# Performance work log

Measured on AMD Instinct MI355X. Metric: run time of the kernel, lower is better.

Reference implementation:

```python
import jax, jax.numpy as jnp
import numpy as np

B, S, D, H, FF = 4, 2048, 512, 8, 2048
HD = D // H
WINDOW = 64  # local attention half-window in rank space
EPS = 1e-5


def _layer_norm(v, g, b):
    m = jnp.mean(v, axis=-1, keepdims=True)
    var = jnp.mean(jnp.square(v - m), axis=-1, keepdims=True)
    return (v - m) / jnp.sqrt(var + EPS) * g + b


def setup_inputs() -> dict:
    key = jax.random.key(0)
    ks = jax.random.split(key, 10)
    sc = 0.02
    x = jax.random.normal(ks[0], (B, S, D), jnp.float32)
    padding_mask = jnp.zeros((B, S), dtype=bool)
    i = jnp.arange(S)
    local = jnp.abs(i[:, None] - i[None, :]) <= WINDOW
    glob = (i[:, None] == 0) | (i[None, :] == 0)  # global spectrum token at pos 0
    attn_mask = jnp.where(local | glob, 0.0, -jnp.inf).astype(jnp.float32)
    return {
        "x": x,
        "padding_mask": padding_mask,
        "attn_mask": attn_mask,
        "in_proj_w": jax.random.normal(ks[1], (3 * D, D), jnp.float32) * sc,
        "in_proj_b": jnp.zeros((3 * D,), jnp.float32),
        "out_proj_w": jax.random.normal(ks[2], (D, D), jnp.float32) * sc,
        "out_proj_b": jnp.zeros((D,), jnp.float32),
        "ln1_g": jnp.ones((D,), jnp.float32),
        "ln1_b": jnp.zeros((D,), jnp.float32),
        "ln2_g": jnp.ones((D,), jnp.float32),
        "ln2_b": jnp.zeros((D,), jnp.float32),
        "ff_w1": jax.random.normal(ks[3], (FF, D), jnp.float32) * sc,
        "ff_b1": jnp.zeros((FF,), jnp.float32),
        "ff_w2": jax.random.normal(ks[4], (D, FF), jnp.float32) * sc,
        "ff_b2": jnp.zeros((D,), jnp.float32),
    }


def reference(x, padding_mask, attn_mask, in_proj_w, in_proj_b, out_proj_w,
              out_proj_b, ln1_g, ln1_b, ln2_g, ln2_b, ff_w1, ff_b1, ff_w2, ff_b2):
    # pre-LN attention
    a = _layer_norm(x, ln1_g, ln1_b)
    qkv = a @ in_proj_w.T + in_proj_b  # [B,S,3D]
    q, k, v = jnp.split(qkv, 3, axis=-1)
    to_heads = lambda t: t.reshape(B, S, H, HD).transpose(0, 2, 1, 3)
    q, k, v = to_heads(q), to_heads(k), to_heads(v)
    scores = jnp.einsum('bhqd,bhkd->bhqk', q, k) * (HD ** -0.5)
    # float attn_mask path: key_padding_mask converted to additive -inf floats
    kpm = jnp.where(padding_mask, -jnp.inf, 0.0).astype(scores.dtype)
    scores = scores + attn_mask[None, None, :, :] + kpm[:, None, None, :]
    p = jax.nn.softmax(scores, axis=-1)
    o = jnp.einsum('bhqk,bhkd->bhqd', p, v).transpose(0, 2, 1, 3).reshape(B, S, D)
    o = o @ out_proj_w.T + out_proj_b
    x = x + o  # residual (dropout = 0)
    # pre-LN feed-forward with exact GELU (torch nn.GELU default)
    f = _layer_norm(x, ln2_g, ln2_b)
    f = jax.nn.gelu(f @ ff_w1.T + ff_b1, approximate=False) @ ff_w2.T + ff_b2
    return x + f
```

## Files before the change

kernel.cpp:

```cpp
#include <hip/hip_runtime.h>
#include <hip/hip_bf16.h>
#include <math.h>

namespace {

constexpr int kB = 4, kS = 2048, kD = 512, kH = 8, kFF = 2048;
constexpr int kM = kB * kS;
constexpr int kHD = kD / kH;
constexpr int kWin = 64;

typedef __attribute__((ext_vector_type(8))) short short8;
typedef __attribute__((ext_vector_type(4))) float f32x4;

__device__ __forceinline__ float bf2f(__hip_bfloat16 v) { return __bfloat162float(v); }
__device__ __forceinline__ __hip_bfloat16 f2bf(float v) { return __float2bfloat16(v); }
__device__ __forceinline__ int iclamp(int v, int lo, int hi) { return v < lo ? lo : (v > hi ? hi : v); }

__device__ __forceinline__ void async16(const void* g, void* l) {
  __builtin_amdgcn_global_load_lds((const __attribute__((address_space(1))) void*)g,
                                   (__attribute__((address_space(3))) void*)l, 16, 0, 0);
}

__global__ __launch_bounds__(256)
void prep(const float* __restrict__ iw, const float* __restrict__ ow,
          const float* __restrict__ f1, const float* __restrict__ f2,
          __hip_bfloat16* __restrict__ wq, __hip_bfloat16* __restrict__ wo,
          __hip_bfloat16* __restrict__ w1, __hip_bfloat16* __restrict__ w2,
          const float* __restrict__ x, const float* __restrict__ g,
          const float* __restrict__ bta, __hip_bfloat16* __restrict__ a,
          __hip_bfloat16* __restrict__ xb) {
  const int id = blockIdx.x;
  if (id < 3072) {
    const float* s; __hip_bfloat16* d; int base;
    if (id < 768)       { s = iw; d = wq; base = id; }
    else if (id < 1024) { s = ow; d = wo; base = id - 768; }
    else if (id < 2048) { s = f1; d = w1; base = id - 1024; }
    else                { s = f2; d = w2; base = id - 2048; }
    int i = base * 1024 + threadIdx.x * 4;
    float4 v = *(const float4*)(s + i);
    union { __hip_bfloat16 h[4]; uint2 u; } t;
    t.h[0] = f2bf(v.x); t.h[1] = f2bf(v.y); t.h[2] = f2bf(v.z); t.h[3] = f2bf(v.w);
    *(uint2*)(d + i) = t.u;
  } else {
    int row = (id - 3072) * 4 + (threadIdx.x >> 6);
    int lane = threadIdx.x & 63;
    const float* xr = x + (size_t)row * kD;
    int c = lane * 8;
    float4 v0 = *(const float4*)(xr + c);
    float4 v1 = *(const float4*)(xr + c + 4);
    union { __hip_bfloat16 h[8]; int4 u; } xr8;
    xr8.h[0] = f2bf(v0.x); xr8.h[1] = f2bf(v0.y); xr8.h[2] = f2bf(v0.z); xr8.h[3] = f2bf(v0.w);
    xr8.h[4] = f2bf(v1.x); xr8.h[5] = f2bf(v1.y); xr8.h[6] = f2bf(v1.z); xr8.h[7] = f2bf(v1.w);
    *(int4*)(xb + (size_t)row * kD + c) = xr8.u;
    float s  = v0.x + v0.y + v0.z + v0.w + v1.x + v1.y + v1.z + v1.w;
    float ss = v0.x*v0.x + v0.y*v0.y + v0.z*v0.z + v0.w*v0.w
             + v1.x*v1.x + v1.y*v1.y + v1.z*v1.z + v1.w*v1.w;
#pragma unroll
    for (int o = 32; o > 0; o >>= 1) { s += __shfl_xor(s, o); ss += __shfl_xor(ss, o); }
    float mean = s * (1.0f / kD);
    float inv  = rsqrtf(ss * (1.0f / kD) - mean * mean + 1e-5f);
    float4 g0 = *(const float4*)(g + c),   g1 = *(const float4*)(g + c + 4);
    float4 b0 = *(const float4*)(bta + c), b1 = *(const float4*)(bta + c + 4);
    union { __hip_bfloat16 h[8]; int4 u; } t;
    t.h[0] = f2bf((v0.x - mean) * inv * g0.x + b0.x);
    t.h[1] = f2bf((v0.y - mean) * inv * g0.y + b0.y);
    t.h[2] = f2bf((v0.z - mean) * inv * g0.z + b0.z);
    t.h[3] = f2bf((v0.w - mean) * inv * g0.w + b0.w);
    t.h[4] = f2bf((v1.x - mean) * inv * g1.x + b1.x);
    t.h[5] = f2bf((v1.y - mean) * inv * g1.y + b1.y);
    t.h[6] = f2bf((v1.z - mean) * inv * g1.z + b1.z);
    t.h[7] = f2bf((v1.w - mean) * inv * g1.w + b1.w);
    *(int4*)(a + (size_t)row * kD + c) = t.u;
  }
}

__global__ __launch_bounds__(256)
void ln_rows_bf(const __hip_bfloat16* __restrict__ x, const float* __restrict__ g,
                const float* __restrict__ bta, __hip_bfloat16* __restrict__ out) {
  int row = blockIdx.x * 4 + (threadIdx.x >> 6);
  int lane = threadIdx.x & 63;
  int c = lane * 8;
  union { short8 v; __hip_bfloat16 hh[8]; } u;
  u.v = *(const short8*)(x + (size_t)row * kD + c);
  float f[8];
  float s = 0.f, ss = 0.f;
#pragma unroll
  for (int i = 0; i < 8; ++i) { f[i] = bf2f(u.hh[i]); s += f[i]; ss += f[i] * f[i]; }
#pragma unroll
  for (int o = 32; o > 0; o >>= 1) { s += __shfl_xor(s, o); ss += __shfl_xor(ss, o); }
  float mean = s * (1.0f / kD);
  float inv  = rsqrtf(ss * (1.0f / kD) - mean * mean + 1e-5f);
  float4 g0 = *(const float4*)(g + c),   g1 = *(const float4*)(g + c + 4);
  float4 b0 = *(const float4*)(bta + c), b1 = *(const float4*)(bta + c + 4);
  union { __hip_bfloat16 h[8]; int4 v; } t;
  t.h[0] = f2bf((f[0] - mean) * inv * g0.x + b0.x);
  t.h[1] = f2bf((f[1] - mean) * inv * g0.y + b0.y);
  t.h[2] = f2bf((f[2] - mean) * inv * g0.z + b0.z);
  t.h[3] = f2bf((f[3] - mean) * inv * g0.w + b0.w);
  t.h[4] = f2bf((f[4] - mean) * inv * g1.x + b1.x);
  t.h[5] = f2bf((f[5] - mean) * inv * g1.y + b1.y);
  t.h[6] = f2bf((f[6] - mean) * inv * g1.z + b1.z);
  t.h[7] = f2bf((f[7] - mean) * inv * g1.w + b1.w);
  *(int4*)(out + (size_t)row * kD + c) = t.v;
}

__global__ __launch_bounds__(64)
void attn_tile(const __hip_bfloat16* __restrict__ qkv, const __hip_bfloat16* __restrict__ vt,
               __hip_bfloat16* __restrict__ o) {
  const int bh = blockIdx.x;
  const int b = bh >> 3, h = bh & 7;
  const int lane = threadIdx.x;

  __shared__ float smem_f[2048];
  __shared__ float qs0[kHD];
  __hip_bfloat16* Pt = (__hip_bfloat16*)smem_f;

  const __hip_bfloat16* base = qkv + (size_t)b * kS * (3 * kD);
  const __hip_bfloat16* vt_bh = vt + (size_t)(b * kH + h) * kHD * kS;

  if (blockIdx.y == 0) {
    qs0[lane] = bf2f(base[h * kHD + lane]) * 0.125f;
    __syncthreads();
    float m = -1e30f;
    for (int kk = lane; kk < kS; kk += 64) {
      const short8* kp = (const short8*)(base + (size_t)kk * (3 * kD) + kD + h * kHD);
      float s = 0.f;
#pragma unroll
      for (int cc = 0; cc < 8; ++cc) {
        union { short8 v; __hip_bfloat16 hh[8]; } u;
        u.v = kp[cc];
#pragma unroll
        for (int d = 0; d < 8; ++d) s += qs0[cc * 8 + d] * bf2f(u.hh[d]);
      }
      smem_f[kk] = s;
      m = fmaxf(m, s);
    }
#pragma unroll
    for (int off = 32; off > 0; off >>= 1) m = fmaxf(m, __shfl_xor(m, off));
    float ls = 0.f;
    __syncthreads();
    for (int kk = lane; kk < kS; kk += 64) {
      float e = __expf(smem_f[kk] - m);
      smem_f[kk] = e;
      ls += e;
    }
#pragma unroll
    for (int off = 32; off > 0; off >>= 1) ls += __shfl_xor(ls, off);
    __syncthreads();
    float a = 0.f;
    const __hip_bfloat16* vr = vt_bh + (size_t)lane * kS;
    for (int c = 0; c < kS / 8; ++c) {
      union { short8 v; __hip_bfloat16 hh[8]; } u;
      u.v = *(const short8*)(vr + c * 8);
#pragma unroll
      for (int j = 0; j < 8; ++j) a += smem_f[c * 8 + j] * bf2f(u.hh[j]);
    }
    o[(size_t)(b * kS) * kD + h * kHD + lane] = f2bf(a / ls);
    return;
  }

  const int tq = blockIdx.y - 1;
  const int quad = lane >> 4, col = lane & 15;
  const int q0 = tq * 16;
  const int kbase = q0 - kWin;

  short8 aq0, aq1;
  {
    const __hip_bfloat16* qrow = base + (size_t)(q0 + col) * (3 * kD) + h * kHD + quad * 8;
    aq0 = *(const short8*)qrow;
    aq1 = *(const short8*)(qrow + 32);
  }

  f32x4 sc[10];
#pragma unroll
  for (int t = 0; t < 10; ++t) {
    int krow = (t < 9) ? iclamp(kbase + t * 16 + col, 0, kS - 1) : col;
    const short8* kp = (const short8*)(base + (size_t)krow * (3 * kD) + kD + h * kHD + quad * 8);
    f32x4 a = (f32x4){0.f, 0.f, 0.f, 0.f};
    a = __builtin_amdgcn_mfma_f32_16x16x32_bf16(aq0, kp[0], a, 0, 0, 0);
    a = __builtin_amdgcn_mfma_f32_16x16x32_bf16(aq1, kp[4], a, 0, 0, 0);
    sc[t] = a;
  }

  float rowmax[4] = {-1e30f, -1e30f, -1e30f, -1e30f};
#pragma unroll
  for (int t = 0; t < 10; ++t) {
#pragma unroll
    for (int r = 0; r < 4; ++r) {
      int q = q0 + quad * 4 + r;
      bool valid;
      if (t < 9) {
        int k = kbase + t * 16 + col;
        valid = (k >= 0) && (k < kS) && ((q - k <= kWin && k - q <= kWin) || k == 0);
      } else {
        valid = (col == 0) && (kbase > 0);
      }
      float s = valid ? sc[t][r] * 0.125f : -1e30f;
      sc[t][r] = s;
      rowmax[r] = fmaxf(rowmax[r], s);
    }
  }
#pragma unroll
  for (int r = 0; r < 4; ++r)
#pragma unroll
    for (int off = 1; off < 16; off <<= 1)
      rowmax[r] = fmaxf(rowmax[r], __shfl_xor(rowmax[r], off));

  float rowsum[4] = {0.f, 0.f, 0.f, 0.f};
#pragma unroll
  for (int t = 0; t < 10; ++t)
#pragma unroll
    for (int r = 0; r < 4; ++r) {
      float e = __expf(sc[t][r] - rowmax[r]);
      sc[t][r] = e;
      rowsum[r] += e;
    }
#pragma unroll
  for (int r = 0; r < 4; ++r)
#pragma unroll
    for (int off = 1; off < 16; off <<= 1)
      rowsum[r] += __shfl_xor(rowsum[r], off);

#pragma unroll
  for (int t = 0; t < 10; ++t) {
    union { ushort u[4]; unsigned long long ll; } pk;
#pragma unroll
    for (int r = 0; r < 4; ++r) {
      __hip_bfloat16 hv = f2bf(sc[t][r]);
      pk.u[r] = *(ushort*)&hv;
    }
    *(unsigned long long*)&Pt[(t * 16 + col) * 20 + quad * 4] = pk.ll;
  }
  __syncthreads();

  f32x4 oacc[4];
#pragma unroll
  for (int n = 0; n < 4; ++n) oacc[n] = (f32x4){0.f, 0.f, 0.f, 0.f};

#pragma unroll
  for (int c = 0; c < 5; ++c) {
    union { short s[8]; short8 v; } pa;
#pragma unroll
    for (int j = 0; j < 8; ++j) pa.s[j] = *(const short*)&Pt[(c * 32 + quad * 8 + j) * 20 + col];
    const int kc = c * 32 + quad * 8;
    const int kstart = (kc < 144) ? iclamp(kbase + kc, 0, kS - 8) : (kc - 144);
#pragma unroll
    for (int n = 0; n < 4; ++n) {
      short8 vb = *(const short8*)(vt_bh + (size_t)(n * 16 + col) * kS + kstart);
      oacc[n] = __builtin_amdgcn_mfma_f32_16x16x32_bf16(pa.v, vb, oacc[n], 0, 0, 0);
    }
  }

#pragma unroll
  for (int n = 0; n < 4; ++n)
#pragma unroll
    for (int r = 0; r < 4; ++r) {
      int q = q0 + quad * 4 + r;
      if (q == 0) continue;
      o[(size_t)(b * kS + q) * kD + h * kHD + n * 16 + col] = f2bf(oacc[n][r] / rowsum[r]);
    }
}

template <int TN, int NB, int EPI, int WVT, typename OT, typename RT>
__global__ __launch_bounds__(256, 4)
void gemm_bt(const __hip_bfloat16* __restrict__ A, const __hip_bfloat16* __restrict__ W,
             const float* __restrict__ bias, const RT* __restrict__ resid,
             OT* __restrict__ C, __hip_bfloat16* __restrict__ vt, int Ndim, int K) {
  constexpr int NF = TN / 32;
  __shared__ __hip_bfloat16 As[128 * 64];
  __shared__ __hip_bfloat16 Ws[TN * 64];

  const int id = blockIdx.x;
  const int rr = id & 7, tt = id >> 3;
  const int nb = tt % NB, mb = (tt / NB) * 8 + rr;

  const int tid = threadIdx.x;
  const int lane = tid & 63, w = tid >> 6;
  const int wm = w >> 1, wn = w & 1;
  const int quad = lane >> 4, mrow = lane & 15;
  const int m0 = mb * 128, n0 = nb * TN;

  const int lrow = lane >> 3;
  const int lcol = ((lane & 7) ^ lrow) << 3;

  f32x4 acc[4][NF];
#pragma unroll
  for (int i = 0; i < 4; ++i)
#pragma unroll
    for (int j = 0; j < NF; ++j) acc[i][j] = (f32x4){0.f, 0.f, 0.f, 0.f};

  for (int kt = 0; kt < K; kt += 64) {
#pragma unroll
    for (int it = 0; it < 4; ++it) {
      int c = w * 4 + it;
      async16(A + (size_t)(m0 + c * 8 + lrow) * K + kt + lcol, &As[c * 512]);
    }
#pragma unroll
    for (int it = 0; it < NF; ++it) {
      int c = w * NF + it;
      async16(W + (size_t)(n0 + c * 8 + lrow) * K + kt + lcol, &Ws[c * 512]);
    }
    __syncthreads();
#pragma unroll
    for (int kk = 0; kk < 64; kk += 32) {
      const int ch = (kk >> 3) + quad;
      const int sw = (ch ^ (mrow & 7)) << 3;
      short8 af[4], wf[NF];
#pragma unroll
      for (int i = 0; i < 4; ++i)
        af[i] = *(const short8*)&As[(wm * 64 + i * 16 + mrow) * 64 + sw];
#pragma unroll
      for (int j = 0; j < NF; ++j)
        wf[j] = *(const short8*)&Ws[(wn * (TN / 2) + j * 16 + mrow) * 64 + sw];
#pragma unroll
      for (int i = 0; i < 4; ++i)
#pragma unroll
        for (int j = 0; j < NF; ++j)
          acc[i][j] = __builtin_amdgcn_mfma_f32_16x16x32_bf16(af[i], wf[j], acc[i][j], 0, 0, 0);
    }
    __syncthreads();
  }

  if constexpr (WVT) {
    if (n0 >= 1024) {
      __hip_bfloat16* Ls = As;
      const int bb = m0 >> 11, ss0 = m0 & (kS - 1);
      const int n0v = n0 - 1024;
#pragma unroll
      for (int p = 0; p < 2; ++p) {
        __syncthreads();
#pragma unroll
        for (int jj = 0; jj < 2; ++jj) {
          int j = p * 2 + jj;
          int lr = wn * 32 + jj * 16 + mrow;
          float bs = bias[1024 + n0v + wn * 64 + j * 16 + mrow];
#pragma unroll
          for (int i = 0; i < 4; ++i) {
            int tok = wm * 64 + i * 16 + quad * 4;
            int tw = tok ^ ((lr & 15) << 3);
            union { __hip_bfloat16 h[4]; unsigned long long u; } pk;
#pragma unroll
            for (int r = 0; r < 4; ++r) pk.h[r] = f2bf(acc[i][j][r] + bs);
            *(unsigned long long*)&Ls[lr * 128 + tw] = pk.u;
          }
        }
        __syncthreads();
#pragma unroll
        for (int i2 = 0; i2 < 4; ++i2) {
          int c = i2 * 256 + tid;
          int lr = c >> 4, off = (c & 15) << 3;
          int tw = off ^ ((lr & 15) << 3);
          short8 v = *(const short8*)&Ls[lr * 128 + tw];
          int colv = (lr >> 5) * 64 + p * 32 + (lr & 31);
          *(short8*)(vt + (size_t)(bb * 512 + n0v + colv) * kS + ss0 + off) = v;
        }
      }
      return;
    }
  }

#pragma unroll
  for (int i = 0; i < 4; ++i) {
#pragma unroll
    for (int r = 0; r < 4; ++r) {
      int row = m0 + wm * 64 + i * 16 + quad * 4 + r;
#pragma unroll
      for (int j = 0; j < NF; ++j) {
        int col = n0 + wn * (TN / 2) + j * 16 + mrow;
        float v = acc[i][j][r] + bias[col];
        if (EPI == 1) v = 0.5f * v * (1.0f + erff(v * 0.70710678118f));
        if (EPI == 3) v += bf2f(((const __hip_bfloat16*)resid)[(size_t)row * Ndim + col]);
        if constexpr (__is_same(OT, float)) C[(size_t)row * Ndim + col] = v;
        else                                C[(size_t)row * Ndim + col] = f2bf(v);
      }
    }
  }
}

}

extern "C" void kernel_launch(void* const* d_in, const int* in_sizes, int n_in,
                              void* d_out, int out_size, void* d_ws, size_t ws_size,
                              hipStream_t stream) {
  const float* x          = (const float*)d_in[0];
  const float* in_proj_w  = (const float*)d_in[3];
  const float* in_proj_b  = (const float*)d_in[4];
  const float* out_proj_w = (const float*)d_in[5];
  const float* out_proj_b = (const float*)d_in[6];
  const float* ln1_g      = (const float*)d_in[7];
  const float* ln1_b      = (const float*)d_in[8];
  const float* ln2_g      = (const float*)d_in[9];
  const float* ln2_b      = (const float*)d_in[10];
  const float* ff_w1      = (const float*)d_in[11];
  const float* ff_b1      = (const float*)d_in[12];
  const float* ff_w2      = (const float*)d_in[13];
  const float* ff_b2      = (const float*)d_in[14];
  float* out = (float*)d_out;

  char* ws = (char*)d_ws;
  size_t off = 0;
  auto carve = [&](size_t bytes) { char* p = ws + off; off += (bytes + 255) & ~(size_t)255; return p; };
  __hip_bfloat16* wqkv_bf = (__hip_bfloat16*)carve((size_t)3 * kD * kD * 2);
  __hip_bfloat16* wout_bf = (__hip_bfloat16*)carve((size_t)kD * kD * 2);
  __hip_bfloat16* wff1_bf = (__hip_bfloat16*)carve((size_t)kFF * kD * 2);
  __hip_bfloat16* wff2_bf = (__hip_bfloat16*)carve((size_t)kD * kFF * 2);
  __hip_bfloat16* a_bf    = (__hip_bfloat16*)carve((size_t)kM * kD * 2);
  __hip_bfloat16* x_bf    = (__hip_bfloat16*)carve((size_t)kM * kD * 2);
  __hip_bfloat16* qkv_bf  = (__hip_bfloat16*)carve((size_t)kM * 3 * kD * 2);
  __hip_bfloat16* vt      = (__hip_bfloat16*)carve((size_t)kM * kD * 2);
  __hip_bfloat16* o_bf    = (__hip_bfloat16*)carve((size_t)kM * kD * 2);
  __hip_bfloat16* r1b     = (__hip_bfloat16*)carve((size_t)kM * kD * 2);
  __hip_bfloat16* ln2_bf  = (__hip_bfloat16*)carve((size_t)kM * kD * 2);
  __hip_bfloat16* ff1_bf  = (__hip_bfloat16*)carve((size_t)kM * kFF * 2);

  prep<<<5120, 256, 0, stream>>>(in_proj_w, out_proj_w, ff_w1, ff_w2,
                                 wqkv_bf, wout_bf, wff1_bf, wff2_bf,
                                 x, ln1_g, ln1_b, a_bf, x_bf);
  gemm_bt<128, 12, 0, 1, __hip_bfloat16, float><<<64 * 12, 256, 0, stream>>>(
      a_bf, wqkv_bf, in_proj_b, nullptr, qkv_bf, vt, 3 * kD, kD);
  attn_tile<<<dim3(kB * kH, kS / 16 + 1), 64, 0, stream>>>(qkv_bf, vt, o_bf);
  gemm_bt<64, 8, 3, 0, __hip_bfloat16, __hip_bfloat16><<<64 * 8, 256, 0, stream>>>(
      o_bf, wout_bf, out_proj_b, x_bf, r1b, nullptr, kD, kD);
  ln_rows_bf<<<kM / 4, 256, 0, stream>>>(r1b, ln2_g, ln2_b, ln2_bf);
  gemm_bt<128, 16, 1, 0, __hip_bfloat16, float><<<64 * 16, 256, 0, stream>>>(
      ln2_bf, wff1_bf, ff_b1, nullptr, ff1_bf, nullptr, kFF, kD);
  gemm_bt<64, 8, 3, 0, float, __hip_bfloat16><<<64 * 8, 256, 0, stream>>>(
      ff1_bf, wff2_bf, ff_b2, r1b, out, nullptr, kD, kFF);
}
```

Before: 266.7 us.

## Pack four attention tiles per block, parallelize global row, shrink M tile for N=512 GEMMs

The attention kernel now launches 256-thread blocks in which each of the four waves handles its own 16-query tile, with a private LDS slice so the block-wide barrier is dropped. The global-token row (query 0) is split across four waves with cross-wave max, sum and partial-output reductions, which removes a long serial 64-thread tail. The GEMM template gains an M-tile parameter, and the out-projection and FF2 GEMMs use 64x64 tiles so they launch twice as many blocks. The aim is better CU occupancy and a shorter critical path, at the cost of lower per-block reuse in the smaller GEMM tiles.

```diff
diff --git a/kernel.cpp b/kernel.cpp
--- a/kernel.cpp
+++ b/kernel.cpp
@@ -104,65 +104,91 @@
   *(int4*)(out + (size_t)row * kD + c) = t.v;
 }
 
-__global__ __launch_bounds__(64)
+__global__ __launch_bounds__(256)
 void attn_tile(const __hip_bfloat16* __restrict__ qkv, const __hip_bfloat16* __restrict__ vt,
                __hip_bfloat16* __restrict__ o) {
   const int bh = blockIdx.x;
   const int b = bh >> 3, h = bh & 7;
-  const int lane = threadIdx.x;
-
-  __shared__ float smem_f[2048];
-  __shared__ float qs0[kHD];
-  __hip_bfloat16* Pt = (__hip_bfloat16*)smem_f;
+  const int tid = threadIdx.x;
+  const int lane = tid & 63, w = tid >> 6;
+
+  __shared__ alignas(16) char smem[4 * 160 * 20 * 2];
 
   const __hip_bfloat16* base = qkv + (size_t)b * kS * (3 * kD);
   const __hip_bfloat16* vt_bh = vt + (size_t)(b * kH + h) * kHD * kS;
 
   if (blockIdx.y == 0) {
-    qs0[lane] = bf2f(base[h * kHD + lane]) * 0.125f;
-    __syncthreads();
+    float* sc   = (float*)smem;
+    float* qs   = sc + 2048;
+    float* redm = qs + 64;
+    float* reds = redm + 4;
+    float* part = reds + 4;
+    if (tid < kHD) qs[tid] = bf2f(base[h * kHD + tid]) * 0.125f;
+    __syncthreads();
+
     float m = -1e30f;
-    for (int kk = lane; kk < kS; kk += 64) {
-      const short8* kp = (const short8*)(base + (size_t)kk * (3 * kD) + kD + h * kHD);
+#pragma unroll
+    for (int it = 0; it < 8; ++it) {
+      int k = it * 256 + tid;
+      const short8* kp = (const short8*)(base + (size_t)k * (3 * kD) + kD + h * kHD);
       float s = 0.f;
 #pragma unroll
       for (int cc = 0; cc < 8; ++cc) {
         union { short8 v; __hip_bfloat16 hh[8]; } u;
         u.v = kp[cc];
 #pragma unroll
-        for (int d = 0; d < 8; ++d) s += qs0[cc * 8 + d] * bf2f(u.hh[d]);
+        for (int d = 0; d < 8; ++d) s += qs[cc * 8 + d] * bf2f(u.hh[d]);
       }
-      smem_f[kk] = s;
+      sc[k] = s;
       m = fmaxf(m, s);
     }
 #pragma unroll
     for (int off = 32; off > 0; off >>= 1) m = fmaxf(m, __shfl_xor(m, off));
+    if (lane == 0) redm[w] = m;
+    __syncthreads();
+    float M = fmaxf(fmaxf(redm[0], redm[1]), fmaxf(redm[2], redm[3]));
+
     float ls = 0.f;
-    __syncthreads();
-    for (int kk = lane; kk < kS; kk += 64) {
-      float e = __expf(smem_f[kk] - m);
-      smem_f[kk] = e;
+#pragma unroll
+    for (int it = 0; it < 8; ++it) {
+      int k = it * 256 + tid;
+      float e = __expf(sc[k] - M);
+      sc[k] = e;
       ls += e;
     }
 #pragma unroll
     for (int off = 32; off > 0; off >>= 1) ls += __shfl_xor(ls, off);
-    __syncthreads();
-    float a = 0.f;
-    const __hip_bfloat16* vr = vt_bh + (size_t)lane * kS;
-    for (int c = 0; c < kS / 8; ++c) {
-      union { short8 v; __hip_bfloat16 hh[8]; } u;
-      u.v = *(const short8*)(vr + c * 8);
-#pragma unroll
-      for (int j = 0; j < 8; ++j) a += smem_f[c * 8 + j] * bf2f(u.hh[j]);
-    }
-    o[(size_t)(b * kS) * kD + h * kHD + lane] = f2bf(a / ls);
+    if (lane == 0) reds[w] = ls;
+    __syncthreads();
+    float L = reds[0] + reds[1] + reds[2] + reds[3];
+
+    float a0 = 0.f, a1 = 0.f;
+    const __hip_bfloat16* vr = vt_bh + (size_t)lane * kS + w * 512;
+#pragma unroll
+    for (int c = 0; c < 64; c += 2) {
+      union { short8 v; __hip_bfloat16 hh[8]; } u0, u1;
+      u0.v = *(const short8*)(vr + c * 8);
+      u1.v = *(const short8*)(vr + c * 8 + 8);
+#pragma unroll
+      for (int j = 0; j < 8; ++j) {
+        a0 += sc[w * 512 + c * 8 + j] * bf2f(u0.hh[j]);
+        a1 += sc[w * 512 + c * 8 + 8 + j] * bf2f(u1.hh[j]);
+      }
+    }
+    part[w * 64 + lane] = a0 + a1;
+    __syncthreads();
+    if (tid < kHD) {
+      float s = part[tid] + part[64 + tid] + part[128 + tid] + part[192 + tid];
+      o[(size_t)(b * kS) * kD + h * kHD + tid] = f2bf(s / L);
+    }
     return;
   }
 
-  const int tq = blockIdx.y - 1;
+  const int tq = (blockIdx.y - 1) * 4 + w;
   const int quad = lane >> 4, col = lane & 15;
   const int q0 = tq * 16;
   const int kbase = q0 - kWin;
+  __hip_bfloat16* Pt = (__hip_bfloat16*)smem + w * 160 * 20;
 
   short8 aq0, aq1;
   {
@@ -231,7 +257,6 @@
     }
     *(unsigned long long*)&Pt[(t * 16 + col) * 20 + quad * 4] = pk.ll;
   }
-  __syncthreads();
 
   f32x4 oacc[4];
 #pragma unroll
@@ -261,13 +286,14 @@
     }
 }
 
-template <int TN, int NB, int EPI, int WVT, typename OT, typename RT>
+template <int TM, int TN, int NB, int EPI, int WVT, typename OT, typename RT>
 __global__ __launch_bounds__(256, 4)
 void gemm_bt(const __hip_bfloat16* __restrict__ A, const __hip_bfloat16* __restrict__ W,
              const float* __restrict__ bias, const RT* __restrict__ resid,
              OT* __restrict__ C, __hip_bfloat16* __restrict__ vt, int Ndim, int K) {
+  constexpr int MI = TM / 32;
   constexpr int NF = TN / 32;
-  __shared__ __hip_bfloat16 As[128 * 64];
+  __shared__ __hip_bfloat16 As[TM * 64];
   __shared__ __hip_bfloat16 Ws[TN * 64];
 
   const int id = blockIdx.x;
@@ -278,21 +304,21 @@
   const int lane = tid & 63, w = tid >> 6;
   const int wm = w >> 1, wn = w & 1;
   const int quad = lane >> 4, mrow = lane & 15;
-  const int m0 = mb * 128, n0 = nb * TN;
+  const int m0 = mb * TM, n0 = nb * TN;
 
   const int lrow = lane >> 3;
   const int lcol = ((lane & 7) ^ lrow) << 3;
 
-  f32x4 acc[4][NF];
-#pragma unroll
-  for (int i = 0; i < 4; ++i)
+  f32x4 acc[MI][NF];
+#pragma unroll
+  for (int i = 0; i < MI; ++i)
 #pragma unroll
     for (int j = 0; j < NF; ++j) acc[i][j] = (f32x4){0.f, 0.f, 0.f, 0.f};
 
   for (int kt = 0; kt < K; kt += 64) {
 #pragma unroll
-    for (int it = 0; it < 4; ++it) {
-      int c = w * 4 + it;
+    for (int it = 0; it < MI; ++it) {
+      int c = w * MI + it;
       async16(A + (size_t)(m0 + c * 8 + lrow) * K + kt + lcol, &As[c * 512]);
     }
 #pragma unroll
@@ -305,15 +331,15 @@
     for (int kk = 0; kk < 64; kk += 32) {
       const int ch = (kk >> 3) + quad;
       const int sw = (ch ^ (mrow & 7)) << 3;
-      short8 af[4], wf[NF];
-#pragma unroll
-      for (int i = 0; i < 4; ++i)
-        af[i] = *(const short8*)&As[(wm * 64 + i * 16 + mrow) * 64 + sw];
+      short8 af[MI], wf[NF];
+#pragma unroll
+      for (int i = 0; i < MI; ++i)
+        af[i] = *(const short8*)&As[(wm * (TM / 2) + i * 16 + mrow) * 64 + sw];
 #pragma unroll
       for (int j = 0; j < NF; ++j)
         wf[j] = *(const short8*)&Ws[(wn * (TN / 2) + j * 16 + mrow) * 64 + sw];
 #pragma unroll
-      for (int i = 0; i < 4; ++i)
+      for (int i = 0; i < MI; ++i)
 #pragma unroll
         for (int j = 0; j < NF; ++j)
           acc[i][j] = __builtin_amdgcn_mfma_f32_16x16x32_bf16(af[i], wf[j], acc[i][j], 0, 0, 0);
@@ -360,10 +386,10 @@
   }
 
 #pragma unroll
-  for (int i = 0; i < 4; ++i) {
+  for (int i = 0; i < MI; ++i) {
 #pragma unroll
     for (int r = 0; r < 4; ++r) {
-      int row = m0 + wm * 64 + i * 16 + quad * 4 + r;
+      int row = m0 + wm * (TM / 2) + i * 16 + quad * 4 + r;
 #pragma unroll
       for (int j = 0; j < NF; ++j) {
         int col = n0 + wn * (TN / 2) + j * 16 + mrow;
@@ -416,14 +442,14 @@
   prep<<<5120, 256, 0, stream>>>(in_proj_w, out_proj_w, ff_w1, ff_w2,
                                  wqkv_bf, wout_bf, wff1_bf, wff2_bf,
                                  x, ln1_g, ln1_b, a_bf, x_bf);
-  gemm_bt<128, 12, 0, 1, __hip_bfloat16, float><<<64 * 12, 256, 0, stream>>>(
+  gemm_bt<128, 128, 12, 0, 1, __hip_bfloat16, float><<<64 * 12, 256, 0, stream>>>(
       a_bf, wqkv_bf, in_proj_b, nullptr, qkv_bf, vt, 3 * kD, kD);
-  attn_tile<<<dim3(kB * kH, kS / 16 + 1), 64, 0, stream>>>(qkv_bf, vt, o_bf);
-  gemm_bt<64, 8, 3, 0, __hip_bfloat16, __hip_bfloat16><<<64 * 8, 256, 0, stream>>>(
+  attn_tile<<<dim3(kB * kH, kS / 64 + 1), 256, 0, stream>>>(qkv_bf, vt, o_bf);
+  gemm_bt<64, 64, 8, 3, 0, __hip_bfloat16, __hip_bfloat16><<<128 * 8, 256, 0, stream>>>(
       o_bf, wout_bf, out_proj_b, x_bf, r1b, nullptr, kD, kD);
   ln_rows_bf<<<kM / 4, 256, 0, stream>>>(r1b, ln2_g, ln2_b, ln2_bf);
-  gemm_bt<128, 16, 1, 0, __hip_bfloat16, float><<<64 * 16, 256, 0, stream>>>(
+  gemm_bt<128, 128, 16, 1, 0, __hip_bfloat16, float><<<64 * 16, 256, 0, stream>>>(
       ln2_bf, wff1_bf, ff_b1, nullptr, ff1_bf, nullptr, kFF, kD);
-  gemm_bt<64, 8, 3, 0, float, __hip_bfloat16><<<64 * 8, 256, 0, stream>>>(
+  gemm_bt<64, 64, 8, 3, 0, float, __hip_bfloat16><<<128 * 8, 256, 0, stream>>>(
       ff1_bf, wff2_bf, ff_b2, r1b, out, nullptr, kD, kFF);
 }
```

After: 239.1 us. -10.3%, faster.
